# Kernel tuning notes

Measured on AMD Instinct MI355X. Metric: run time of the kernel, lower is better.

## Reference

```python
import jax, jax.numpy as jnp
import numpy as np

# Module hyperparameters (from init_kwargs)
NUM_NEURONS = 16384
BATCH = 2048  # processed sequentially, sharing neuron state
V_TH0 = 1.0
V_RESET = 0.0
TAU = 20.0
DT = 1.0
ETA = 0.1
NOISE_STD = 0.1
MIN_TH = 0.5
MAX_TH = 2.0
USE_ADAPTIVE = True
STOCHASTIC = True


def setup_inputs() -> dict:
    key = jax.random.key(0)
    k1, k2 = jax.random.split(key)
    input_current = jax.random.normal(k1, (BATCH, NUM_NEURONS), dtype=jnp.float32)
    # stochastic membrane noise, pre-sampled for determinism
    noise = NOISE_STD * jax.random.normal(k2, (BATCH, NUM_NEURONS), dtype=jnp.float32)
    if not STOCHASTIC:
        noise = jnp.zeros_like(noise)
    return {"input_current": input_current, "noise": noise}


def reference(input_current, noise):
    # Faithful to the torch wrapper: each batch row is fed through the SAME
    # LIFNeuronGroup sequentially, carrying membrane potential V and the
    # adaptive threshold V_th across rows -> lax.scan over the batch axis.
    n = input_current.shape[1]
    V0 = jnp.full((n,), V_RESET, dtype=jnp.float32)
    Vth0 = jnp.full((n,), V_TH0, dtype=jnp.float32)

    def step(carry, inp):
        V, Vth = carry
        I, nz = inp
        # leaky integration + noise injection (fused elementwise)
        V = V + (DT / TAU) * (I - V) + nz
        spikes = V >= Vth
        V = jnp.where(spikes, V_RESET, V)
        if USE_ADAPTIVE:
            Vth = jnp.clip(Vth + ETA * spikes.astype(jnp.float32), MIN_TH, MAX_TH)
        return (V, Vth), spikes.astype(jnp.float32)

    (_, _), out_spikes = jax.lax.scan(step, (V0, Vth0), (input_current, noise))
    return out_spikes  # [batch, num_neurons] binary float32
```

## Files before the change

### kernel.cpp

```cpp
#include <hip/hip_runtime.h>


constexpr int N = 16384;
constexpr int T = 2048;
constexpr int U = 4;
constexpr int C = T / U;
constexpr int R = 16;
constexpr int P = 14;

static_assert(C == 512 && R == 16 && P <= R - 2, "schedule geometry");

typedef float f4v __attribute__((ext_vector_type(4)));

__device__ __forceinline__ unsigned lds_off(const void* p) {
    return (unsigned)(size_t)(const __attribute__((address_space(3))) void*)p;
}

__device__ __forceinline__ void dma16(const float* g, unsigned lds) {
    asm volatile(
        "s_mov_b32 m0, %1\n\t"
        "global_load_lds_dwordx4 %0, off\n\t"
        "s_mov_b32 m0, -1"
        :: "v"(g), "s"(lds) : "memory");
}

#define WAITV(K) asm volatile("s_waitcnt vmcnt(" #K ")" ::: "memory")

__global__
__attribute__((amdgpu_flat_work_group_size(64, 64)))
void TorchLIFNeuronGroup_85152021610615_kernel(const float* __restrict__ I,
                                               const float* __restrict__ Z,
                                               float* __restrict__ O) {
    #pragma clang fp contract(off)
    __shared__ __align__(16) float ring[R][2][U][64];
    __shared__ __align__(16) float sbuf[U][64];

    const int lane = threadIdx.x;
    const int g    = lane >> 4;
    const int c4   = (lane & 15) << 2;
    const size_t laneOff = (size_t)g * N + c4;

    const float* ipfx = I + (size_t)blockIdx.x * 64 + laneOff;
    const float* zpfx = Z + (size_t)blockIdx.x * 64 + laneOff;
    float*       opfx = O + (size_t)blockIdx.x * 64 + laneOff;

    const unsigned rb = lds_off(&ring[0][0][0][0]);

    float V   = 0.0f;
    float Vth = 1.0f;

    #pragma unroll
    for (int c = 0; c < P; ++c) {
        dma16(ipfx + (size_t)(c * U) * N, rb + (unsigned)(c * 2 + 0) * 1024u);
        dma16(zpfx + (size_t)(c * U) * N, rb + (unsigned)(c * 2 + 1) * 1024u);
    }

    int t = 0;

#define STAGE(d, K, PF)                                                       \
    {                                                                         \
        WAITV(K);                                                             \
        _Pragma("unroll")                                                     \
        for (int u = 0; u < U; ++u) {                                         \
            float Iv = ring[d][0][u][lane];                                   \
            float Zv = ring[d][1][u][lane];                                   \
            float dd = Iv - V;                                                \
            float v1 = V + 0.05f * dd;                            \
            float v2 = v1 + Zv;                                               \
            bool  s  = (v2 >= Vth);                                           \
            V = s ? 0.0f : v2;                                                \
            float nth = fminf(fmaxf(Vth + 0.1f, 0.5f), 2.0f);                 \
            Vth = s ? nth : Vth;                                              \
            sbuf[u][lane] = s ? 1.0f : 0.0f;                                  \
        }                                                                     \
        {                                                                     \
            f4v sv = *reinterpret_cast<const f4v*>(&sbuf[g][c4]);             \
            __builtin_nontemporal_store(                                      \
                sv, reinterpret_cast<f4v*>(opfx + (size_t)t * N));            \
        }                                                                     \
        if (PF) {                                                             \
            dma16(ipfx + (size_t)(t + P * U) * N,                             \
                  rb + (unsigned)((((d) + P) & (R - 1)) * 2 + 0) * 1024u);    \
            dma16(zpfx + (size_t)(t + P * U) * N,                             \
                  rb + (unsigned)((((d) + P) & (R - 1)) * 2 + 1) * 1024u);    \
        }                                                                     \
        __builtin_amdgcn_sched_barrier(0);                                    \
        t += U;                                                               \
    }

    STAGE(0, 26, 1)  STAGE(1, 27, 1)  STAGE(2, 28, 1)  STAGE(3, 29, 1)
    STAGE(4, 30, 1)  STAGE(5, 31, 1)  STAGE(6, 32, 1)  STAGE(7, 33, 1)
    STAGE(8, 34, 1)  STAGE(9, 35, 1)  STAGE(10, 36, 1) STAGE(11, 37, 1)
    STAGE(12, 38, 1) STAGE(13, 39, 1) STAGE(14, 39, 1) STAGE(15, 39, 1)

    for (int it = 1; it <= 30; ++it) {
        STAGE(0, 39, 1)  STAGE(1, 39, 1)  STAGE(2, 39, 1)  STAGE(3, 39, 1)
        STAGE(4, 39, 1)  STAGE(5, 39, 1)  STAGE(6, 39, 1)  STAGE(7, 39, 1)
        STAGE(8, 39, 1)  STAGE(9, 39, 1)  STAGE(10, 39, 1) STAGE(11, 39, 1)
        STAGE(12, 39, 1) STAGE(13, 39, 1) STAGE(14, 39, 1) STAGE(15, 39, 1)
    }

    STAGE(0, 39, 1)  STAGE(1, 39, 1)
    STAGE(2, 39, 0)  STAGE(3, 37, 0)  STAGE(4, 35, 0)  STAGE(5, 33, 0)
    STAGE(6, 31, 0)  STAGE(7, 29, 0)  STAGE(8, 27, 0)  STAGE(9, 25, 0)
    STAGE(10, 23, 0) STAGE(11, 21, 0) STAGE(12, 19, 0) STAGE(13, 17, 0)
    STAGE(14, 15, 0) STAGE(15, 13, 0)

#undef STAGE
}

extern "C" void kernel_launch(void* const* d_in, const int* in_sizes, int n_in,
                              void* d_out, int out_size, void* d_ws, size_t ws_size,
                              hipStream_t stream) {
    const float* input_current = (const float*)d_in[0];
    const float* noise         = (const float*)d_in[1];
    float* out                 = (float*)d_out;

    TorchLIFNeuronGroup_85152021610615_kernel<<<N / 64, 64, 0, stream>>>(
        input_current, noise, out);
}
```

Before: 330.2 us.

## Software-pipeline LDS reads and output stores one stage ahead

```diff
diff --git a/kernel.cpp b/kernel.cpp
--- a/kernel.cpp
+++ b/kernel.cpp
@@ -33,7 +33,7 @@
                                                float* __restrict__ O) {
     #pragma clang fp contract(off)
     __shared__ __align__(16) float ring[R][2][U][64];
-    __shared__ __align__(16) float sbuf[U][64];
+    __shared__ __align__(16) float sbuf[2][U][64];
 
     const int lane = threadIdx.x;
     const int g    = lane >> 4;
@@ -48,22 +48,37 @@
 
     float V   = 0.0f;
     float Vth = 1.0f;
+    float rr[2][8];
 
     #pragma unroll
     for (int c = 0; c < P; ++c) {
         dma16(ipfx + (size_t)(c * U) * N, rb + (unsigned)(c * 2 + 0) * 1024u);
         dma16(zpfx + (size_t)(c * U) * N, rb + (unsigned)(c * 2 + 1) * 1024u);
     }
+    WAITV(26);
+    #pragma unroll
+    for (int u = 0; u < U; ++u) {
+        rr[0][u]     = ring[0][0][u][lane];
+        rr[0][4 + u] = ring[0][1][u][lane];
+    }
 
     int t = 0;
 
-#define STAGE(d, K, PF)                                                       \
+#define STAGE_BODY(d, PF, LD, ST)                                             \
     {                                                                         \
-        WAITV(K);                                                             \
+        f4v sv{};                                                             \
+        if (ST) sv = *reinterpret_cast<const f4v*>(&sbuf[((d) + 1) & 1][g][c4]); \
+        if (LD) {                                                             \
+            _Pragma("unroll")                                                 \
+            for (int u = 0; u < U; ++u) {                                     \
+                rr[((d) + 1) & 1][u]     = ring[((d) + 1) & (R - 1)][0][u][lane]; \
+                rr[((d) + 1) & 1][4 + u] = ring[((d) + 1) & (R - 1)][1][u][lane]; \
+            }                                                                 \
+        }                                                                     \
         _Pragma("unroll")                                                     \
         for (int u = 0; u < U; ++u) {                                         \
-            float Iv = ring[d][0][u][lane];                                   \
-            float Zv = ring[d][1][u][lane];                                   \
+            float Iv = rr[(d) & 1][u];                                        \
+            float Zv = rr[(d) & 1][4 + u];                                    \
             float dd = Iv - V;                                                \
             float v1 = V + 0.05f * dd;                            \
             float v2 = v1 + Zv;                                               \
@@ -71,13 +86,10 @@
             V = s ? 0.0f : v2;                                                \
             float nth = fminf(fmaxf(Vth + 0.1f, 0.5f), 2.0f);                 \
             Vth = s ? nth : Vth;                                              \
-            sbuf[u][lane] = s ? 1.0f : 0.0f;                                  \
+            sbuf[(d) & 1][u][lane] = s ? 1.0f : 0.0f;                         \
         }                                                                     \
-        {                                                                     \
-            f4v sv = *reinterpret_cast<const f4v*>(&sbuf[g][c4]);             \
-            __builtin_nontemporal_store(                                      \
-                sv, reinterpret_cast<f4v*>(opfx + (size_t)t * N));            \
-        }                                                                     \
+        if (ST) __builtin_nontemporal_store(                                  \
+                    sv, reinterpret_cast<f4v*>(opfx + (size_t)(t - U) * N));  \
         if (PF) {                                                             \
             dma16(ipfx + (size_t)(t + P * U) * N,                             \
                   rb + (unsigned)((((d) + P) & (R - 1)) * 2 + 0) * 1024u);    \
@@ -88,25 +100,39 @@
         t += U;                                                               \
     }
 
-    STAGE(0, 26, 1)  STAGE(1, 27, 1)  STAGE(2, 28, 1)  STAGE(3, 29, 1)
-    STAGE(4, 30, 1)  STAGE(5, 31, 1)  STAGE(6, 32, 1)  STAGE(7, 33, 1)
-    STAGE(8, 34, 1)  STAGE(9, 35, 1)  STAGE(10, 36, 1) STAGE(11, 37, 1)
-    STAGE(12, 38, 1) STAGE(13, 39, 1) STAGE(14, 39, 1) STAGE(15, 39, 1)
+#define STAGE(d, K, PF, LD, ST) { WAITV(K); STAGE_BODY(d, PF, LD, ST) }
+
+    STAGE(0, 24, 1, 1, 0)  STAGE(1, 24, 1, 1, 1)  STAGE(2, 25, 1, 1, 1)
+    STAGE(3, 26, 1, 1, 1)  STAGE(4, 27, 1, 1, 1)  STAGE(5, 28, 1, 1, 1)
+    STAGE(6, 29, 1, 1, 1)  STAGE(7, 30, 1, 1, 1)  STAGE(8, 31, 1, 1, 1)
+    STAGE(9, 32, 1, 1, 1)  STAGE(10, 33, 1, 1, 1) STAGE(11, 34, 1, 1, 1)
+    STAGE(12, 35, 1, 1, 1) STAGE(13, 36, 1, 1, 1) STAGE(14, 36, 1, 1, 1)
+    STAGE(15, 36, 1, 1, 1)
 
     for (int it = 1; it <= 30; ++it) {
-        STAGE(0, 39, 1)  STAGE(1, 39, 1)  STAGE(2, 39, 1)  STAGE(3, 39, 1)
-        STAGE(4, 39, 1)  STAGE(5, 39, 1)  STAGE(6, 39, 1)  STAGE(7, 39, 1)
-        STAGE(8, 39, 1)  STAGE(9, 39, 1)  STAGE(10, 39, 1) STAGE(11, 39, 1)
-        STAGE(12, 39, 1) STAGE(13, 39, 1) STAGE(14, 39, 1) STAGE(15, 39, 1)
+        STAGE(0, 36, 1, 1, 1)  STAGE(1, 36, 1, 1, 1)  STAGE(2, 36, 1, 1, 1)
+        STAGE(3, 36, 1, 1, 1)  STAGE(4, 36, 1, 1, 1)  STAGE(5, 36, 1, 1, 1)
+        STAGE(6, 36, 1, 1, 1)  STAGE(7, 36, 1, 1, 1)  STAGE(8, 36, 1, 1, 1)
+        STAGE(9, 36, 1, 1, 1)  STAGE(10, 36, 1, 1, 1) STAGE(11, 36, 1, 1, 1)
+        STAGE(12, 36, 1, 1, 1) STAGE(13, 36, 1, 1, 1) STAGE(14, 36, 1, 1, 1)
+        STAGE(15, 36, 1, 1, 1)
     }
 
-    STAGE(0, 39, 1)  STAGE(1, 39, 1)
-    STAGE(2, 39, 0)  STAGE(3, 37, 0)  STAGE(4, 35, 0)  STAGE(5, 33, 0)
-    STAGE(6, 31, 0)  STAGE(7, 29, 0)  STAGE(8, 27, 0)  STAGE(9, 25, 0)
-    STAGE(10, 23, 0) STAGE(11, 21, 0) STAGE(12, 19, 0) STAGE(13, 17, 0)
-    STAGE(14, 15, 0) STAGE(15, 13, 0)
+    STAGE(0, 36, 1, 1, 1)   STAGE(1, 36, 1, 1, 1)   STAGE(2, 36, 0, 1, 1)
+    STAGE(3, 34, 0, 1, 1)   STAGE(4, 32, 0, 1, 1)   STAGE(5, 30, 0, 1, 1)
+    STAGE(6, 28, 0, 1, 1)   STAGE(7, 26, 0, 1, 1)   STAGE(8, 24, 0, 1, 1)
+    STAGE(9, 22, 0, 1, 1)   STAGE(10, 20, 0, 1, 1)  STAGE(11, 18, 0, 1, 1)
+    STAGE(12, 16, 0, 1, 1)  STAGE(13, 14, 0, 1, 1)  STAGE(14, 12, 0, 1, 1)
+    STAGE_BODY(15, 0, 0, 1)
+
+    {
+        f4v sv = *reinterpret_cast<const f4v*>(&sbuf[1][g][c4]);
+        __builtin_nontemporal_store(
+            sv, reinterpret_cast<f4v*>(opfx + (size_t)(T - U) * N));
+    }
 
 #undef STAGE
+#undef STAGE_BODY
 }
 
 extern "C" void kernel_launch(void* const* d_in, const int* in_sizes, int n_in,
```

New measurement: 314.9 us. 1.05x faster.
